# Performance work log

Hardware: AMD Instinct MI355X
Metric: run time of the kernel (lower is better)

The kernel has to match this reference:

```python
import jax, jax.numpy as jnp
import numpy as np

B, K, S, HS = 32, 8, 512, 256


def setup_inputs() -> dict:
    key = jax.random.key(0)
    ks = jax.random.split(key, 12)
    sc = 1.0 / np.sqrt(HS)
    return {
        "rem_fea": jax.random.normal(ks[0], (B, S, HS), jnp.float32),
        "ret_fea": jax.random.normal(ks[1], (B, K, S, HS), jnp.float32),
        "Wr": jax.random.normal(ks[2], (HS, HS), jnp.float32) * sc,
        "br": jax.random.normal(ks[3], (HS,), jnp.float32) * sc,
        "Wt": jax.random.normal(ks[4], (HS, HS), jnp.float32) * sc,
        "bt": jax.random.normal(ks[5], (HS,), jnp.float32) * sc,
        "W1": jax.random.normal(ks[6], (K, HS, HS), jnp.float32) * sc,
        "b1": jax.random.normal(ks[7], (K, HS), jnp.float32) * sc,
        "W2": jax.random.normal(ks[8], (K, HS, HS), jnp.float32) * sc,
        "b2": jax.random.normal(ks[9], (K, HS), jnp.float32) * sc,
    }


def reference(rem_fea, ret_fea, Wr, br, Wt, bt, W1, b1, W2, b2):
    # ---- MACRouter ----
    rem_lin = rem_fea @ Wr + br                       # [B,S,hs]
    ret_lin = jnp.einsum("bksd,de->bkse", ret_fea, Wt) + bt  # [B,K,S,hs]
    avg_rem = rem_lin.mean(axis=1)                    # [B,hs]
    avg_ret = ret_lin.mean(axis=2)                    # [B,K,hs]
    scores = jnp.einsum("bd,bkd->bk", avg_rem, avg_ret)
    routing = jax.nn.softmax(scores, axis=1)          # [B,K]
    # ---- K dense experts (batched over K) ----
    h = jax.nn.relu(jnp.einsum("bksd,kde->bkse", ret_fea, W1) + b1[None, :, None, :])
    expert_outs = jnp.einsum("bksd,kde->bkse", h, W2) + b2[None, :, None, :]
    # ---- weighted sum over experts ----
    gen_fea = jnp.einsum("bksd,bk->bsd", expert_outs, routing)
    return gen_fea
```

## Files before the change

kernel.cpp:

```cpp
#include <hip/hip_runtime.h>
#include <hip/hip_bf16.h>

typedef __attribute__((ext_vector_type(8))) short bf16x8;
typedef __attribute__((ext_vector_type(4))) float f32x4;

constexpr int Bb = 32, Kk = 8, Ss = 512, HS = 256;
constexpr int SUB = 32;
constexpr int NST = Ss / SUB;
constexpr int SUB_BYTES = SUB * HS * 2;
constexpr int MT = 64;

__device__ __forceinline__ unsigned short f2bf(float f) {
  unsigned int u = __builtin_bit_cast(unsigned int, f);
  u = (u + 0x7FFFu + ((u >> 16) & 1u)) >> 16;
  return (unsigned short)u;
}

__device__ __forceinline__ void gload_lds16(const void* g, void* l) {
  __builtin_amdgcn_global_load_lds((const __attribute__((address_space(1))) void*)g,
                                   (__attribute__((address_space(3))) void*)l, 16, 0, 0);
}

__global__ void prep(const float* __restrict__ rem, const float* __restrict__ ret,
                     const float* __restrict__ W1, const float* __restrict__ W2,
                     unsigned short* __restrict__ W1p, unsigned short* __restrict__ W2p,
                     char* __restrict__ swz, float* __restrict__ partial_ret,
                     float* __restrict__ partial_rem) {
  int blk = blockIdx.x, t = threadIdx.x;
  if (blk < 512) {
    const float* W = (blk < 256) ? W1 : W2;
    unsigned short* Wp = (blk < 256) ? W1p : W2p;
    int idx = (blk & 255) * 256 + t;
    int lane = idx & 63, nt = (idx >> 6) & 15, kk = (idx >> 10) & 7, k = idx >> 13;
    const float* src = W + ((size_t)k * HS + kk * 32 + ((lane >> 4) * 8)) * HS + nt * 16 + (lane & 15);
    unsigned short* dst = Wp + (size_t)idx * 8;
#pragma unroll
    for (int i = 0; i < 8; ++i) dst[i] = f2bf(src[(size_t)i * HS]);
    return;
  }
  blk -= 512;
  const float* src;
  float* pdst;
  char* dst = nullptr;
  if (blk < Bb * Kk * NST) {
    int st = blk & 15, bk = blk >> 4;
    src = ret + ((size_t)bk * Ss + st * SUB) * HS;
    pdst = partial_ret + (size_t)blk * HS;
    if (swz) dst = swz + (size_t)blk * SUB_BYTES;
  } else {
    int rid = blk - Bb * Kk * NST;
    int st = rid & 15, b = rid >> 4;
    src = rem + ((size_t)b * Ss + st * SUB) * HS;
    pdst = partial_rem + (size_t)rid * HS;
  }
  f32x4 acc = {0.f, 0.f, 0.f, 0.f};
#pragma unroll
  for (int j = 0; j < 8; ++j) {
    int f = j * 256 + t;
    int row = f >> 6, c4 = f & 63;
    f32x4 v = *reinterpret_cast<const f32x4*>(src + (size_t)row * HS + c4 * 4);
    acc += v;
    if (dst) {
      union { unsigned short h[4]; unsigned long long u; } pk;
      pk.h[0] = f2bf(v[0]); pk.h[1] = f2bf(v[1]); pk.h[2] = f2bf(v[2]); pk.h[3] = f2bf(v[3]);
      int off = (c4 >> 5) * 8192 + row * 256 + ((((c4 & 31) >> 1) ^ (row & 7)) * 16) + (c4 & 1) * 8;
      *reinterpret_cast<unsigned long long*>(dst + off) = pk.u;
    }
  }
  __shared__ f32x4 red[256];
  red[t] = acc;
  __syncthreads();
  if (t < 64) {
    f32x4 s = red[t] + red[t + 64] + red[t + 128] + red[t + 192];
    *reinterpret_cast<f32x4*>(pdst + t * 4) = s;
  }
}

template <int SRC>
__launch_bounds__(512, 1)
__global__ void experts_kernel(const float* __restrict__ ret, const char* __restrict__ ret_swz,
                               const unsigned short* __restrict__ W1p,
                               const unsigned short* __restrict__ W2p,
                               const float* __restrict__ b1, const float* __restrict__ b2,
                               const float* __restrict__ partial_ret,
                               const float* __restrict__ partial_rem,
                               const float* __restrict__ Wr, const float* __restrict__ br,
                               const float* __restrict__ Wt, const float* __restrict__ bt,
                               float* __restrict__ out) {
  __shared__ __align__(16) char A_lds[2][2 * SUB_BYTES];
  __shared__ __align__(16) char H_lds[MT * HS * 2];
  __shared__ float srem_sh[HS];
  __shared__ float sret_sh[Kk][HS];
  __shared__ float shred[8];
  __shared__ float scores_sh[Kk];
  __shared__ float routing_sh[Kk];

  const int blk = blockIdx.x;
  const int b = blk >> 3, st64 = blk & 7;
  const int tid = threadIdx.x;
  const int wave = tid >> 6, lane = tid & 63;
  const int l15 = lane & 15, l4 = lane >> 4;
  const int t256 = tid & 255, half = tid >> 8;

  auto stage = [&](int k, int bufi) {
    if constexpr (SRC == 0) {
      const char* tb = ret_swz + ((size_t)((b * Kk + k) * NST + st64 * 2)) * SUB_BYTES;
#pragma unroll
      for (int i = 0; i < 4; ++i) {
        int c = wave + i * 8;
        gload_lds16(tb + c * 1024 + (size_t)lane * 16, A_lds[bufi] + c * 1024);
      }
    } else {
      const float* src = ret + ((size_t)(b * Kk + k) * Ss + st64 * MT) * HS;
#pragma unroll
      for (int j = 0; j < 8; ++j) {
        int f = j * 512 + tid;
        int row = f >> 6, c4 = f & 63;
        f32x4 v = *reinterpret_cast<const f32x4*>(src + (size_t)row * HS + c4 * 4);
        union { unsigned short h[4]; unsigned long long u; } pk;
        pk.h[0] = f2bf(v[0]); pk.h[1] = f2bf(v[1]); pk.h[2] = f2bf(v[2]); pk.h[3] = f2bf(v[3]);
        int off = (row >> 5) * 16384 + (c4 >> 5) * 8192 + (row & 31) * 256 +
                  ((((c4 & 31) >> 1) ^ (row & 7)) * 16) + (c4 & 1) * 8;
        *reinterpret_cast<unsigned long long*>(A_lds[bufi] + off) = pk.u;
      }
    }
  };

  stage(0, 0);

  {
#pragma unroll
    for (int kk = 0; kk < 4; ++kk) {
      int k = half * 4 + kk;
      float sk = 0.f;
      for (int st = 0; st < NST; ++st)
        sk += partial_ret[((size_t)((b * Kk + k) * NST + st)) * HS + t256];
      sret_sh[k][t256] = sk;
    }
    if (half == 1) {
      float s_ = 0.f;
      for (int st = 0; st < NST; ++st)
        s_ += partial_rem[((size_t)(b * NST + st)) * HS + t256];
      srem_sh[t256] = s_;
    }
    __syncthreads();

    float rl = 0.f;
    float tl[4] = {0.f, 0.f, 0.f, 0.f};
    for (int e = 0; e < HS; ++e) {
      float wr = Wr[(size_t)e * HS + t256];
      float wt = Wt[(size_t)e * HS + t256];
      rl += srem_sh[e] * wr;
#pragma unroll
      for (int kk = 0; kk < 4; ++kk) tl[kk] += sret_sh[half * 4 + kk][e] * wt;
    }
    rl = rl * (1.f / Ss) + br[t256];

    for (int kk = 0; kk < 4; ++kk) {
      float p = rl * (tl[kk] * (1.f / Ss) + bt[t256]);
#pragma unroll
      for (int off = 32; off; off >>= 1) p += __shfl_down(p, off);
      if (lane == 0) shred[wave] = p;
      __syncthreads();
      if (tid == 0) scores_sh[kk] = shred[0] + shred[1] + shred[2] + shred[3];
      else if (tid == 256) scores_sh[4 + kk] = shred[4] + shred[5] + shred[6] + shred[7];
      __syncthreads();
    }
    if (tid == 0) {
      float mx = scores_sh[0];
      for (int k = 1; k < Kk; ++k) mx = fmaxf(mx, scores_sh[k]);
      float ssum = 0.f, ev[Kk];
      for (int k = 0; k < Kk; ++k) { ev[k] = expf(scores_sh[k] - mx); ssum += ev[k]; }
      for (int k = 0; k < Kk; ++k) routing_sh[k] = ev[k] / ssum;
    }
  }
  asm volatile("s_waitcnt vmcnt(0) lgkmcnt(0)\n\ts_barrier" ::: "memory");

  f32x4 out_acc[4][2];
#pragma unroll
  for (int m = 0; m < 4; ++m)
#pragma unroll
    for (int n = 0; n < 2; ++n) out_acc[m][n] = {0.f, 0.f, 0.f, 0.f};
  const f32x4 zero4 = {0.f, 0.f, 0.f, 0.f};

  int buf = 0;
  for (int k = 0; k < Kk; ++k) {
    if (k + 1 < Kk) stage(k + 1, buf ^ 1);

    const unsigned short* W1k = W1p + (size_t)k * 65536;
    bf16x8 w1f[8][2];
#pragma unroll
    for (int kk = 0; kk < 8; ++kk)
#pragma unroll
      for (int m = 0; m < 2; ++m)
        w1f[kk][m] = *reinterpret_cast<const bf16x8*>(
            W1k + ((size_t)(kk * 16 + wave * 2 + m) * 64 + lane) * 8);

    f32x4 accH[2][4];
#pragma unroll
    for (int m = 0; m < 2; ++m)
#pragma unroll
      for (int n = 0; n < 4; ++n) accH[m][n] = zero4;

#pragma unroll
    for (int kk = 0; kk < 8; ++kk) {
      bf16x8 aA[4];
#pragma unroll
      for (int n = 0; n < 4; ++n) {
        int srow = n * 16 + l15;
        int r5 = srow & 31;
        int off = (srow >> 5) * 16384 + (kk >> 2) * 8192 + r5 * 256 +
                  ((((kk & 3) * 4 + l4) ^ (r5 & 7)) * 16);
        aA[n] = *reinterpret_cast<const bf16x8*>(A_lds[buf] + off);
      }
#pragma unroll
      for (int m = 0; m < 2; ++m)
#pragma unroll
        for (int n = 0; n < 4; ++n)
          accH[m][n] = __builtin_amdgcn_mfma_f32_16x16x32_bf16(w1f[kk][m], aA[n], accH[m][n], 0, 0, 0);
    }

    {
      float r = routing_sh[k];
#pragma unroll
      for (int m = 0; m < 2; ++m) {
        int e0 = wave * 32 + m * 16 + l4 * 4;
        float4 b1v = *reinterpret_cast<const float4*>(b1 + k * HS + e0);
#pragma unroll
        for (int n = 0; n < 4; ++n) {
          int srow = n * 16 + l15;
          union { unsigned short h[4]; unsigned long long u; } pk;
          pk.h[0] = f2bf(fmaxf(accH[m][n][0] + b1v.x, 0.f) * r);
          pk.h[1] = f2bf(fmaxf(accH[m][n][1] + b1v.y, 0.f) * r);
          pk.h[2] = f2bf(fmaxf(accH[m][n][2] + b1v.z, 0.f) * r);
          pk.h[3] = f2bf(fmaxf(accH[m][n][3] + b1v.w, 0.f) * r);
          int boff = srow * 512 + ((e0 * 2) ^ ((srow & 7) << 4));
          *reinterpret_cast<unsigned long long*>(H_lds + boff) = pk.u;
        }
      }
    }

    const unsigned short* W2k = W2p + (size_t)k * 65536;
    bf16x8 w2f[8][2];
#pragma unroll
    for (int kk = 0; kk < 8; ++kk)
#pragma unroll
      for (int n = 0; n < 2; ++n)
        w2f[kk][n] = *reinterpret_cast<const bf16x8*>(
            W2k + ((size_t)(kk * 16 + wave * 2 + n) * 64 + lane) * 8);

    asm volatile("s_waitcnt lgkmcnt(0)\n\ts_barrier" ::: "memory");

#pragma unroll
    for (int kk = 0; kk < 8; ++kk) {
      bf16x8 aH[4];
#pragma unroll
      for (int m = 0; m < 4; ++m) {
        int r = m * 16 + l15;
        int boff = r * 512 + ((kk * 64 + l4 * 16) ^ ((r & 7) << 4));
        aH[m] = *reinterpret_cast<const bf16x8*>(H_lds + boff);
      }
#pragma unroll
      for (int m = 0; m < 4; ++m)
#pragma unroll
        for (int n = 0; n < 2; ++n)
          out_acc[m][n] = __builtin_amdgcn_mfma_f32_16x16x32_bf16(aH[m], w2f[kk][n], out_acc[m][n], 0, 0, 0);
    }
    asm volatile("s_waitcnt vmcnt(0) lgkmcnt(0)\n\ts_barrier" ::: "memory");
    buf ^= 1;
  }

  float bias2[2];
#pragma unroll
  for (int n = 0; n < 2; ++n) {
    int col = (wave * 2 + n) * 16 + l15;
    float s = 0.f;
#pragma unroll
    for (int k = 0; k < Kk; ++k) s += routing_sh[k] * b2[k * HS + col];
    bias2[n] = s;
  }
#pragma unroll
  for (int m = 0; m < 4; ++m)
#pragma unroll
    for (int i = 0; i < 4; ++i) {
      int row = m * 16 + l4 * 4 + i;
      float* orow = out + ((size_t)b * Ss + st64 * MT + row) * HS;
#pragma unroll
      for (int n = 0; n < 2; ++n)
        orow[(wave * 2 + n) * 16 + l15] = out_acc[m][n][i] + bias2[n];
    }
}

extern "C" void kernel_launch(void* const* d_in, const int* in_sizes, int n_in,
                              void* d_out, int out_size, void* d_ws, size_t ws_size,
                              hipStream_t stream) {
  const float* rem = (const float*)d_in[0];
  const float* ret = (const float*)d_in[1];
  const float* Wr  = (const float*)d_in[2];
  const float* br  = (const float*)d_in[3];
  const float* Wt  = (const float*)d_in[4];
  const float* bt  = (const float*)d_in[5];
  const float* W1  = (const float*)d_in[6];
  const float* b1  = (const float*)d_in[7];
  const float* W2  = (const float*)d_in[8];
  const float* b2  = (const float*)d_in[9];
  float* out = (float*)d_out;

  char* w = (char*)d_ws;
  unsigned short* W1p = (unsigned short*)w;
  unsigned short* W2p = (unsigned short*)(w + (1u << 20));
  float* partial_ret  = (float*)(w + (2u << 20));
  float* partial_rem  = (float*)(w + (6u << 20));
  char*  ret_swz      = w + (7u << 20);

  bool full = ws_size >= ((size_t)71 << 20);

  prep<<<512 + Bb * Kk * NST + Bb * NST, 256, 0, stream>>>(rem, ret, W1, W2, W1p, W2p,
                                                           full ? ret_swz : nullptr,
                                                           partial_ret, partial_rem);
  if (full)
    experts_kernel<0><<<Bb * (Ss / MT), 512, 0, stream>>>(ret, ret_swz, W1p, W2p, b1, b2,
                                                          partial_ret, partial_rem,
                                                          Wr, br, Wt, bt, out);
  else
    experts_kernel<1><<<Bb * (Ss / MT), 512, 0, stream>>>(ret, nullptr, W1p, W2p, b1, b2,
                                                          partial_ret, partial_rem,
                                                          Wr, br, Wt, bt, out);
}
```

Before: 98.88 us.

## Software-pipeline expert GEMMs with double-buffered H tile to drop mid-loop barrier

Restructures the per-expert loop so GEMM2 of expert k-1 runs in the same iteration as GEMM1 of expert k, using a double-buffered H tile in LDS. This removes one barrier per iteration and lets the two GEMMs' MFMA and memory work interleave. The routing scratch arrays are aliased into the first H buffer so the extra buffer fits in LDS. W2 fragments are now loaded per kk inside GEMM2 instead of all up front, which lowers register pressure but may expose global load latency.

```diff
diff --git a/kernel.cpp b/kernel.cpp
--- a/kernel.cpp
+++ b/kernel.cpp
@@ -88,12 +88,13 @@
                                const float* __restrict__ Wt, const float* __restrict__ bt,
                                float* __restrict__ out) {
   __shared__ __align__(16) char A_lds[2][2 * SUB_BYTES];
-  __shared__ __align__(16) char H_lds[MT * HS * 2];
-  __shared__ float srem_sh[HS];
-  __shared__ float sret_sh[Kk][HS];
-  __shared__ float shred[8];
-  __shared__ float scores_sh[Kk];
+  __shared__ __align__(16) char H_lds[2][MT * HS * 2];
   __shared__ float routing_sh[Kk];
+
+  float* srem_sh = reinterpret_cast<float*>(H_lds[0]);
+  float (*sret_sh)[HS] = reinterpret_cast<float(*)[HS]>(H_lds[0] + 1024);
+  float* shred = reinterpret_cast<float*>(H_lds[0] + 1024 + 8192);
+  float* scores_sh = reinterpret_cast<float*>(H_lds[0] + 1024 + 8192 + 32);
 
   const int blk = blockIdx.x;
   const int b = blk >> 3, st64 = blk & 7;
@@ -183,25 +184,23 @@
     for (int n = 0; n < 2; ++n) out_acc[m][n] = {0.f, 0.f, 0.f, 0.f};
   const f32x4 zero4 = {0.f, 0.f, 0.f, 0.f};
 
-  int buf = 0;
-  for (int k = 0; k < Kk; ++k) {
-    if (k + 1 < Kk) stage(k + 1, buf ^ 1);
-
+  bf16x8 w1f[8][2];
+  auto load_w1f = [&](int k) {
     const unsigned short* W1k = W1p + (size_t)k * 65536;
-    bf16x8 w1f[8][2];
 #pragma unroll
     for (int kk = 0; kk < 8; ++kk)
 #pragma unroll
       for (int m = 0; m < 2; ++m)
         w1f[kk][m] = *reinterpret_cast<const bf16x8*>(
             W1k + ((size_t)(kk * 16 + wave * 2 + m) * 64 + lane) * 8);
-
+  };
+
+  auto gemm1_epi = [&](int k, int abuf, int hbuf) {
     f32x4 accH[2][4];
 #pragma unroll
     for (int m = 0; m < 2; ++m)
 #pragma unroll
       for (int n = 0; n < 4; ++n) accH[m][n] = zero4;
-
 #pragma unroll
     for (int kk = 0; kk < 8; ++kk) {
       bf16x8 aA[4];
@@ -211,7 +210,7 @@
         int r5 = srow & 31;
         int off = (srow >> 5) * 16384 + (kk >> 2) * 8192 + r5 * 256 +
                   ((((kk & 3) * 4 + l4) ^ (r5 & 7)) * 16);
-        aA[n] = *reinterpret_cast<const bf16x8*>(A_lds[buf] + off);
+        aA[n] = *reinterpret_cast<const bf16x8*>(A_lds[abuf] + off);
       }
 #pragma unroll
       for (int m = 0; m < 2; ++m)
@@ -219,56 +218,64 @@
         for (int n = 0; n < 4; ++n)
           accH[m][n] = __builtin_amdgcn_mfma_f32_16x16x32_bf16(w1f[kk][m], aA[n], accH[m][n], 0, 0, 0);
     }
-
-    {
-      float r = routing_sh[k];
-#pragma unroll
-      for (int m = 0; m < 2; ++m) {
-        int e0 = wave * 32 + m * 16 + l4 * 4;
-        float4 b1v = *reinterpret_cast<const float4*>(b1 + k * HS + e0);
-#pragma unroll
-        for (int n = 0; n < 4; ++n) {
-          int srow = n * 16 + l15;
-          union { unsigned short h[4]; unsigned long long u; } pk;
-          pk.h[0] = f2bf(fmaxf(accH[m][n][0] + b1v.x, 0.f) * r);
-          pk.h[1] = f2bf(fmaxf(accH[m][n][1] + b1v.y, 0.f) * r);
-          pk.h[2] = f2bf(fmaxf(accH[m][n][2] + b1v.z, 0.f) * r);
-          pk.h[3] = f2bf(fmaxf(accH[m][n][3] + b1v.w, 0.f) * r);
-          int boff = srow * 512 + ((e0 * 2) ^ ((srow & 7) << 4));
-          *reinterpret_cast<unsigned long long*>(H_lds + boff) = pk.u;
-        }
-      }
-    }
-
+    float r = routing_sh[k];
+#pragma unroll
+    for (int m = 0; m < 2; ++m) {
+      int e0 = wave * 32 + m * 16 + l4 * 4;
+      float4 b1v = *reinterpret_cast<const float4*>(b1 + k * HS + e0);
+#pragma unroll
+      for (int n = 0; n < 4; ++n) {
+        int srow = n * 16 + l15;
+        union { unsigned short h[4]; unsigned long long u; } pk;
+        pk.h[0] = f2bf(fmaxf(accH[m][n][0] + b1v.x, 0.f) * r);
+        pk.h[1] = f2bf(fmaxf(accH[m][n][1] + b1v.y, 0.f) * r);
+        pk.h[2] = f2bf(fmaxf(accH[m][n][2] + b1v.z, 0.f) * r);
+        pk.h[3] = f2bf(fmaxf(accH[m][n][3] + b1v.w, 0.f) * r);
+        int boff = srow * 512 + ((e0 * 2) ^ ((srow & 7) << 4));
+        *reinterpret_cast<unsigned long long*>(H_lds[hbuf] + boff) = pk.u;
+      }
+    }
+  };
+
+  auto gemm2 = [&](int k, int hbuf) {
     const unsigned short* W2k = W2p + (size_t)k * 65536;
-    bf16x8 w2f[8][2];
-#pragma unroll
-    for (int kk = 0; kk < 8; ++kk)
-#pragma unroll
-      for (int n = 0; n < 2; ++n)
-        w2f[kk][n] = *reinterpret_cast<const bf16x8*>(
-            W2k + ((size_t)(kk * 16 + wave * 2 + n) * 64 + lane) * 8);
-
-    asm volatile("s_waitcnt lgkmcnt(0)\n\ts_barrier" ::: "memory");
-
 #pragma unroll
     for (int kk = 0; kk < 8; ++kk) {
-      bf16x8 aH[4];
+      bf16x8 aH[4], bW[2];
 #pragma unroll
       for (int m = 0; m < 4; ++m) {
         int r = m * 16 + l15;
         int boff = r * 512 + ((kk * 64 + l4 * 16) ^ ((r & 7) << 4));
-        aH[m] = *reinterpret_cast<const bf16x8*>(H_lds + boff);
-      }
+        aH[m] = *reinterpret_cast<const bf16x8*>(H_lds[hbuf] + boff);
+      }
+#pragma unroll
+      for (int n = 0; n < 2; ++n)
+        bW[n] = *reinterpret_cast<const bf16x8*>(
+            W2k + ((size_t)(kk * 16 + wave * 2 + n) * 64 + lane) * 8);
 #pragma unroll
       for (int m = 0; m < 4; ++m)
 #pragma unroll
         for (int n = 0; n < 2; ++n)
-          out_acc[m][n] = __builtin_amdgcn_mfma_f32_16x16x32_bf16(aH[m], w2f[kk][n], out_acc[m][n], 0, 0, 0);
-    }
+          out_acc[m][n] = __builtin_amdgcn_mfma_f32_16x16x32_bf16(aH[m], bW[n], out_acc[m][n], 0, 0, 0);
+    }
+  };
+
+  {
+    stage(1, 1);
+    load_w1f(0);
+    gemm1_epi(0, 0, 0);
+  }
+  asm volatile("s_waitcnt vmcnt(0) lgkmcnt(0)\n\ts_barrier" ::: "memory");
+
+  for (int p = 1; p < Kk; ++p) {
+    if (p + 1 < Kk) stage(p + 1, (p + 1) & 1);
+    load_w1f(p);
+    gemm2(p - 1, (p - 1) & 1);
+    gemm1_epi(p, p & 1, p & 1);
     asm volatile("s_waitcnt vmcnt(0) lgkmcnt(0)\n\ts_barrier" ::: "memory");
-    buf ^= 1;
-  }
+  }
+
+  gemm2(Kk - 1, (Kk - 1) & 1);
 
   float bias2[2];
 #pragma unroll
```

New measurement: 111.6 us. 12.8% more time.
